# Optimization experiments

Measured on AMD Instinct MI355X. Metric: run time of the kernel, lower is better.

The kernel has to match this reference:

```python
import jax, jax.numpy as jnp
import numpy as np

N = 16777216  # batch*A*width*height (flat anchor-score vector)
BINS = 10
LOSS_WEIGHT = 1.0


def setup_inputs() -> dict:
    key = jax.random.key(0)
    k1, k2, k3 = jax.random.split(key, 3)
    pred = jax.random.normal(k1, (N,), dtype=jnp.float32)          # IoU logits
    target = jax.random.uniform(k2, (N,), dtype=jnp.float32)       # IoU targets in [0,1]
    label_weight = (jax.random.uniform(k3, (N,)) > 0.3).astype(jnp.float32)  # 1=valid, 0=ignore
    return {"pred": pred, "target": target, "label_weight": label_weight, "bins": BINS}


def reference(pred, target, label_weight, bins):
    # target is detached in the original module
    target = jax.lax.stop_gradient(target)
    # gradient norm g = |sigmoid(pred).detach() - target|, lies in [0,1]
    g = jnp.abs(jax.lax.stop_gradient(jax.nn.sigmoid(pred)) - target)
    valid = label_weight > 0
    validf = valid.astype(jnp.float32)
    tot = jnp.maximum(jnp.sum(validf), 1.0)

    # edges are i/bins with last edge nudged by 1e-6, so bin = floor(g*bins) clipped to bins-1
    bin_idx = jnp.clip((g * bins).astype(jnp.int32), 0, bins - 1)
    counts = jax.ops.segment_sum(validf, bin_idx, num_segments=bins)  # per-bin valid counts
    n = jnp.sum(counts > 0).astype(jnp.float32)                        # number of nonempty bins
    counts_safe = jnp.maximum(counts, 1.0)
    w_per_bin = jnp.where(counts > 0, tot / counts_safe, 0.0) / jnp.maximum(n, 1.0)
    weights = jnp.where(valid, w_per_bin[bin_idx], 0.0)

    # weighted BCE-with-logits, reduction='sum', stable form: logaddexp(0,x) - x*z
    bce = jnp.logaddexp(0.0, pred) - pred * target
    loss = jnp.sum(weights * bce) / tot
    return loss * LOSS_WEIGHT
```

## Files before the change

### kernel.cpp

```cpp
#include <hip/hip_runtime.h>

#define BINS 10
#define REPLICAS 16
#define NBLOCKS 2048
#define NTHREADS 256


typedef float vfloat4 __attribute__((ext_vector_type(4)));

__global__ __launch_bounds__(NTHREADS, 4)
void ghm_pass1(const float* __restrict__ pred,
               const float* __restrict__ target,
               const float* __restrict__ lw,
               float* __restrict__ rep_sums,
               unsigned int* __restrict__ rep_cnts,
               int n)
{
    __shared__ float ls[BINS];
    __shared__ unsigned int lc[BINS];
    if (threadIdx.x < BINS) { ls[threadIdx.x] = 0.0f; lc[threadIdx.x] = 0u; }

    float s0=0.f,s1=0.f,s2=0.f,s3=0.f,s4=0.f,s5=0.f,s6=0.f,s7=0.f,s8=0.f,s9=0.f;
    unsigned long long cpk = 0ull;

#define SBIN(B, S) { (S) += (bi_ == (B)) ? bce_ : 0.0f; }
#define PROC(P, T, W) do {                                                     \
    float p_ = (P), t_ = (T);                                                  \
    float ap_ = fabsf(p_);                                                     \
    float q_  = __builtin_amdgcn_exp2f(ap_ * -1.4426950408889634f); \
    float r_  = __builtin_amdgcn_rcpf(1.0f + q_);                              \
    float sig_ = (p_ >= 0.0f) ? r_ : (1.0f - r_);                              \
    float g_   = fabsf(sig_ - t_);                                             \
    int bi_ = (int)(g_ * 10.0f);                                               \
    bi_ = bi_ > 9 ? 9 : bi_;                                                   \
    bi_ = ((W) > 0.0f) ? bi_ : 10;              \
    float bce_ = fmaxf(p_, 0.0f)                                               \
               + 0.6931471805599453f * __builtin_amdgcn_logf(1.0f + q_)        \
               - p_ * t_;                                                      \
    cpk += 1ull << (6 * bi_);                                                  \
    SBIN(0,s0) SBIN(1,s1) SBIN(2,s2) SBIN(3,s3) SBIN(4,s4)                     \
    SBIN(5,s5) SBIN(6,s6) SBIN(7,s7) SBIN(8,s8) SBIN(9,s9)                     \
} while (0)
#define PROC4(PV, TV, WV) {                                                    \
    PROC((PV).x, (TV).x, (WV).x);                                              \
    PROC((PV).y, (TV).y, (WV).y);                                              \
    PROC((PV).z, (TV).z, (WV).z);                                              \
    PROC((PV).w, (TV).w, (WV).w); }

    const int n4 = n >> 2;
    const int full = n4 / (NBLOCKS * NTHREADS);
    const vfloat4* p4 = (const vfloat4*)pred;
    const vfloat4* t4 = (const vfloat4*)target;
    const vfloat4* w4 = (const vfloat4*)lw;
    const int gid = blockIdx.x * NTHREADS + threadIdx.x;
    const int stride = NBLOCKS * NTHREADS;

    if (full == 8) {
        const int base = blockIdx.x * 8 * NTHREADS + threadIdx.x;
#define LD(J, PB, TB, WB)                                                      \
        vfloat4 PB = __builtin_nontemporal_load(&p4[base + (J) * NTHREADS]);   \
        vfloat4 TB = __builtin_nontemporal_load(&t4[base + (J) * NTHREADS]);   \
        vfloat4 WB = __builtin_nontemporal_load(&w4[base + (J) * NTHREADS]);
        LD(0, P0, T0, W0) LD(1, P1, T1, W1) LD(2, P2, T2, W2) LD(3, P3, T3, W3)
        LD(4, P4, T4, W4) LD(5, P5, T5, W5) LD(6, P6, T6, W6) LD(7, P7, T7, W7)
        __builtin_amdgcn_sched_barrier(0);
        PROC4(P0, T0, W0);
        PROC4(P1, T1, W1);
        PROC4(P2, T2, W2);
        PROC4(P3, T3, W3);
        PROC4(P4, T4, W4);
        PROC4(P5, T5, W5);
        PROC4(P6, T6, W6);
        PROC4(P7, T7, W7);
#undef LD
    } else {
        if (full >= 2) {
            const int base = blockIdx.x * full * NTHREADS + threadIdx.x;
            vfloat4 pA = __builtin_nontemporal_load(&p4[base]);
            vfloat4 tA = __builtin_nontemporal_load(&t4[base]);
            vfloat4 wA = __builtin_nontemporal_load(&w4[base]);
            vfloat4 pB = __builtin_nontemporal_load(&p4[base + NTHREADS]);
            vfloat4 tB = __builtin_nontemporal_load(&t4[base + NTHREADS]);
            vfloat4 wB = __builtin_nontemporal_load(&w4[base + NTHREADS]);
            __builtin_amdgcn_sched_barrier(0);
            for (int j = 2; j < full; ++j) {
                const int idx = base + j * NTHREADS;
                vfloat4 pC = __builtin_nontemporal_load(&p4[idx]);
                vfloat4 tC = __builtin_nontemporal_load(&t4[idx]);
                vfloat4 wC = __builtin_nontemporal_load(&w4[idx]);
                __builtin_amdgcn_sched_barrier(0);
                PROC4(pA, tA, wA);
                pA = pB; tA = tB; wA = wB;
                pB = pC; tB = tC; wB = wC;
            }
            PROC4(pA, tA, wA);
            PROC4(pB, tB, wB);
        } else if (full == 1) {
            const int base = blockIdx.x * NTHREADS + threadIdx.x;
            vfloat4 pv = p4[base], tv = t4[base], wv = w4[base];
            PROC4(pv, tv, wv);
        }
        for (int i = full * stride + gid; i < n4; i += stride) {
            vfloat4 pv = p4[i], tv = t4[i], wv = w4[i];
            PROC4(pv, tv, wv);
        }
        for (int j = (n4 << 2) + gid; j < n; j += stride) {
            PROC(pred[j], target[j], lw[j]);
        }
    }

    unsigned int c0 = (unsigned int)(cpk       ) & 63u;
    unsigned int c1 = (unsigned int)(cpk >>  6 ) & 63u;
    unsigned int c2 = (unsigned int)(cpk >> 12 ) & 63u;
    unsigned int c3 = (unsigned int)(cpk >> 18 ) & 63u;
    unsigned int c4 = (unsigned int)(cpk >> 24 ) & 63u;
    unsigned int c5 = (unsigned int)(cpk >> 30 ) & 63u;
    unsigned int c6 = (unsigned int)(cpk >> 36 ) & 63u;
    unsigned int c7 = (unsigned int)(cpk >> 42 ) & 63u;
    unsigned int c8 = (unsigned int)(cpk >> 48 ) & 63u;
    unsigned int c9 = (unsigned int)(cpk >> 54 ) & 63u;

#define WREDUCE(S, C) {                                                        \
    _Pragma("unroll")                                                          \
    for (int o_ = 32; o_ > 0; o_ >>= 1) {                                      \
        (S) += __shfl_down((S), o_, 64);                                       \
        (C) += __shfl_down((C), o_, 64);                                       \
    } }
    WREDUCE(s0,c0) WREDUCE(s1,c1) WREDUCE(s2,c2) WREDUCE(s3,c3) WREDUCE(s4,c4)
    WREDUCE(s5,c5) WREDUCE(s6,c6) WREDUCE(s7,c7) WREDUCE(s8,c8) WREDUCE(s9,c9)

    __syncthreads();
    if ((threadIdx.x & 63) == 0) {
        atomicAdd(&ls[0], s0); atomicAdd(&lc[0], c0);
        atomicAdd(&ls[1], s1); atomicAdd(&lc[1], c1);
        atomicAdd(&ls[2], s2); atomicAdd(&lc[2], c2);
        atomicAdd(&ls[3], s3); atomicAdd(&lc[3], c3);
        atomicAdd(&ls[4], s4); atomicAdd(&lc[4], c4);
        atomicAdd(&ls[5], s5); atomicAdd(&lc[5], c5);
        atomicAdd(&ls[6], s6); atomicAdd(&lc[6], c6);
        atomicAdd(&ls[7], s7); atomicAdd(&lc[7], c7);
        atomicAdd(&ls[8], s8); atomicAdd(&lc[8], c8);
        atomicAdd(&ls[9], s9); atomicAdd(&lc[9], c9);
    }
    __syncthreads();
    if (threadIdx.x < BINS) {
        int rep = blockIdx.x & (REPLICAS - 1);
        atomicAdd(&rep_sums[rep * BINS + threadIdx.x], ls[threadIdx.x]);
        atomicAdd(&rep_cnts[rep * BINS + threadIdx.x], lc[threadIdx.x]);
    }
#undef PROC
#undef PROC4
#undef SBIN
#undef WREDUCE
}

__global__ void ghm_finalize(const float* __restrict__ rep_sums,
                             const unsigned int* __restrict__ rep_cnts,
                             float* __restrict__ out)
{
    __shared__ double S[BINS];
    __shared__ unsigned int C[BINS];
    int t = threadIdx.x;
    if (t < BINS) {
        double s = 0.0;
        unsigned int cc = 0u;
        for (int r = 0; r < REPLICAS; ++r) {
            s += (double)rep_sums[r * BINS + t];
            cc += rep_cnts[r * BINS + t];
        }
        S[t] = s;
        C[t] = cc;
    }
    __syncthreads();
    if (t == 0) {
        double n_ne = 0.0;
        for (int b = 0; b < BINS; ++b) if (C[b] > 0u) n_ne += 1.0;
        double nn = n_ne > 1.0 ? n_ne : 1.0;
        double loss = 0.0;
        for (int b = 0; b < BINS; ++b)
            if (C[b] > 0u) loss += S[b] / ((double)C[b] * nn);
        out[0] = (float)loss;
    }
}

extern "C" void kernel_launch(void* const* d_in, const int* in_sizes, int n_in,
                              void* d_out, int out_size, void* d_ws, size_t ws_size,
                              hipStream_t stream)
{
    const float* pred = (const float*)d_in[0];
    const float* target = (const float*)d_in[1];
    const float* lw = (const float*)d_in[2];
    int n = in_sizes[0];

    float* rep_sums = (float*)d_ws;
    unsigned int* rep_cnts =
        (unsigned int*)((char*)d_ws + REPLICAS * BINS * sizeof(float));

    (void)hipMemsetAsync(d_ws, 0, 2 * REPLICAS * BINS * sizeof(float), stream);
    ghm_pass1<<<NBLOCKS, NTHREADS, 0, stream>>>(pred, target, lw,
                                                rep_sums, rep_cnts, n);
    ghm_finalize<<<1, 64, 0, stream>>>(rep_sums, rep_cnts, (float*)d_out);
}
```

Measured before the change: 186.6 us.

## Replace register per-bin accumulators with replicated shared-memory atomic histogram

Each element no longer does ten predicated adds into per-bin register sums plus a packed 64-bit counter. It now issues LDS float atomics into a shared histogram replicated 16 ways by lane. The wave shuffle reductions go away, and the counts become floats, with the finalize kernel adjusted to match. The aim is to cut per-element ALU work and register pressure. The cost is two LDS atomics per valid element, with bank and replica contention (lanes 16 apart share a slot), and float counts lose exactness above 2^24 per slot.

```diff
diff --git a/kernel.cpp b/kernel.cpp
--- a/kernel.cpp
+++ b/kernel.cpp
@@ -1,6 +1,7 @@
 #include <hip/hip_runtime.h>
 
 #define BINS 10
+#define HREP 16
 #define REPLICAS 16
 #define NBLOCKS 2048
 #define NTHREADS 256
@@ -13,17 +14,19 @@
                const float* __restrict__ target,
                const float* __restrict__ lw,
                float* __restrict__ rep_sums,
-               unsigned int* __restrict__ rep_cnts,
+               float* __restrict__ rep_cnts,
                int n)
 {
-    __shared__ float ls[BINS];
-    __shared__ unsigned int lc[BINS];
-    if (threadIdx.x < BINS) { ls[threadIdx.x] = 0.0f; lc[threadIdx.x] = 0u; }
+    __shared__ float hsum[BINS * HREP];
+    __shared__ float hcnt[BINS * HREP];
+    if (threadIdx.x < BINS * HREP) {
+        hsum[threadIdx.x] = 0.0f;
+        hcnt[threadIdx.x] = 0.0f;
+    }
+    __syncthreads();
 
-    float s0=0.f,s1=0.f,s2=0.f,s3=0.f,s4=0.f,s5=0.f,s6=0.f,s7=0.f,s8=0.f,s9=0.f;
-    unsigned long long cpk = 0ull;
+    const int rep_ = threadIdx.x & (HREP - 1);
 
-#define SBIN(B, S) { (S) += (bi_ == (B)) ? bce_ : 0.0f; }
 #define PROC(P, T, W) do {                                                     \
     float p_ = (P), t_ = (T);                                                  \
     float ap_ = fabsf(p_);                                                     \
@@ -33,13 +36,14 @@
     float g_   = fabsf(sig_ - t_);                                             \
     int bi_ = (int)(g_ * 10.0f);                                               \
     bi_ = bi_ > 9 ? 9 : bi_;                                                   \
-    bi_ = ((W) > 0.0f) ? bi_ : 10;              \
     float bce_ = fmaxf(p_, 0.0f)                                               \
                + 0.6931471805599453f * __builtin_amdgcn_logf(1.0f + q_)        \
                - p_ * t_;                                                      \
-    cpk += 1ull << (6 * bi_);                                                  \
-    SBIN(0,s0) SBIN(1,s1) SBIN(2,s2) SBIN(3,s3) SBIN(4,s4)                     \
-    SBIN(5,s5) SBIN(6,s6) SBIN(7,s7) SBIN(8,s8) SBIN(9,s9)                     \
+    if ((W) > 0.0f) {                                                          \
+        int a_ = (bi_ << 4) + rep_;                                            \
+        atomicAdd(&hsum[a_], bce_);                 \
+        atomicAdd(&hcnt[a_], 1.0f);                                            \
+    }                                                                          \
 } while (0)
 #define PROC4(PV, TV, WV) {                                                    \
     PROC((PV).x, (TV).x, (WV).x);                                              \
@@ -109,64 +113,35 @@
         }
     }
 
-    unsigned int c0 = (unsigned int)(cpk       ) & 63u;
-    unsigned int c1 = (unsigned int)(cpk >>  6 ) & 63u;
-    unsigned int c2 = (unsigned int)(cpk >> 12 ) & 63u;
-    unsigned int c3 = (unsigned int)(cpk >> 18 ) & 63u;
-    unsigned int c4 = (unsigned int)(cpk >> 24 ) & 63u;
-    unsigned int c5 = (unsigned int)(cpk >> 30 ) & 63u;
-    unsigned int c6 = (unsigned int)(cpk >> 36 ) & 63u;
-    unsigned int c7 = (unsigned int)(cpk >> 42 ) & 63u;
-    unsigned int c8 = (unsigned int)(cpk >> 48 ) & 63u;
-    unsigned int c9 = (unsigned int)(cpk >> 54 ) & 63u;
-
-#define WREDUCE(S, C) {                                                        \
-    _Pragma("unroll")                                                          \
-    for (int o_ = 32; o_ > 0; o_ >>= 1) {                                      \
-        (S) += __shfl_down((S), o_, 64);                                       \
-        (C) += __shfl_down((C), o_, 64);                                       \
-    } }
-    WREDUCE(s0,c0) WREDUCE(s1,c1) WREDUCE(s2,c2) WREDUCE(s3,c3) WREDUCE(s4,c4)
-    WREDUCE(s5,c5) WREDUCE(s6,c6) WREDUCE(s7,c7) WREDUCE(s8,c8) WREDUCE(s9,c9)
-
-    __syncthreads();
-    if ((threadIdx.x & 63) == 0) {
-        atomicAdd(&ls[0], s0); atomicAdd(&lc[0], c0);
-        atomicAdd(&ls[1], s1); atomicAdd(&lc[1], c1);
-        atomicAdd(&ls[2], s2); atomicAdd(&lc[2], c2);
-        atomicAdd(&ls[3], s3); atomicAdd(&lc[3], c3);
-        atomicAdd(&ls[4], s4); atomicAdd(&lc[4], c4);
-        atomicAdd(&ls[5], s5); atomicAdd(&lc[5], c5);
-        atomicAdd(&ls[6], s6); atomicAdd(&lc[6], c6);
-        atomicAdd(&ls[7], s7); atomicAdd(&lc[7], c7);
-        atomicAdd(&ls[8], s8); atomicAdd(&lc[8], c8);
-        atomicAdd(&ls[9], s9); atomicAdd(&lc[9], c9);
-    }
     __syncthreads();
     if (threadIdx.x < BINS) {
+        float ssum = 0.0f, scnt = 0.0f;
+        const int b16 = threadIdx.x << 4;
+#pragma unroll
+        for (int r = 0; r < HREP; ++r) {
+            ssum += hsum[b16 + r];
+            scnt += hcnt[b16 + r];
+        }
         int rep = blockIdx.x & (REPLICAS - 1);
-        atomicAdd(&rep_sums[rep * BINS + threadIdx.x], ls[threadIdx.x]);
-        atomicAdd(&rep_cnts[rep * BINS + threadIdx.x], lc[threadIdx.x]);
+        atomicAdd(&rep_sums[rep * BINS + threadIdx.x], ssum);
+        atomicAdd(&rep_cnts[rep * BINS + threadIdx.x], scnt);
     }
 #undef PROC
 #undef PROC4
-#undef SBIN
-#undef WREDUCE
 }
 
 __global__ void ghm_finalize(const float* __restrict__ rep_sums,
-                             const unsigned int* __restrict__ rep_cnts,
+                             const float* __restrict__ rep_cnts,
                              float* __restrict__ out)
 {
     __shared__ double S[BINS];
-    __shared__ unsigned int C[BINS];
+    __shared__ double C[BINS];
     int t = threadIdx.x;
     if (t < BINS) {
-        double s = 0.0;
-        unsigned int cc = 0u;
+        double s = 0.0, cc = 0.0;
         for (int r = 0; r < REPLICAS; ++r) {
             s += (double)rep_sums[r * BINS + t];
-            cc += rep_cnts[r * BINS + t];
+            cc += (double)rep_cnts[r * BINS + t];
         }
         S[t] = s;
         C[t] = cc;
@@ -174,11 +149,11 @@
     __syncthreads();
     if (t == 0) {
         double n_ne = 0.0;
-        for (int b = 0; b < BINS; ++b) if (C[b] > 0u) n_ne += 1.0;
+        for (int b = 0; b < BINS; ++b) if (C[b] > 0.0) n_ne += 1.0;
         double nn = n_ne > 1.0 ? n_ne : 1.0;
         double loss = 0.0;
         for (int b = 0; b < BINS; ++b)
-            if (C[b] > 0u) loss += S[b] / ((double)C[b] * nn);
+            if (C[b] > 0.0) loss += S[b] / (C[b] * nn);
         out[0] = (float)loss;
     }
 }
@@ -193,8 +168,7 @@
     int n = in_sizes[0];
 
     float* rep_sums = (float*)d_ws;
-    unsigned int* rep_cnts =
-        (unsigned int*)((char*)d_ws + REPLICAS * BINS * sizeof(float));
+    float* rep_cnts = (float*)((char*)d_ws + REPLICAS * BINS * sizeof(float));
 
     (void)hipMemsetAsync(d_ws, 0, 2 * REPLICAS * BINS * sizeof(float), stream);
     ghm_pass1<<<NBLOCKS, NTHREADS, 0, stream>>>(pred, target, lw,
```

New measurement: 269.4 us. 1.44x slower.

## Replace register select-accumulate histogram with per-thread LDS rows updated by atomics

Applied to the files above, without the earlier changes.

Swaps the ten register accumulators (updated by compare-and-select for every element) and the packed 6-bit count word for a private 11-float-stride row per thread in shared memory, updated with LDS float atomicAdd for both sum and count. Counts become floats, and the finalize kernel reads them as doubles. The sigmoid gradient is also rewritten to pick the target side by sign instead of recomputing 1-r. The change trades ALU select work for two LDS atomics per element and about 22KB of LDS per block, which can lower occupancy and add LDS latency to a kernel that is memory-bound.

```diff
diff --git a/kernel.cpp b/kernel.cpp
--- a/kernel.cpp
+++ b/kernel.cpp
@@ -1,6 +1,7 @@
 #include <hip/hip_runtime.h>
 
 #define BINS 10
+#define ROWW 11
 #define REPLICAS 16
 #define NBLOCKS 2048
 #define NTHREADS 256
@@ -13,33 +14,36 @@
                const float* __restrict__ target,
                const float* __restrict__ lw,
                float* __restrict__ rep_sums,
-               unsigned int* __restrict__ rep_cnts,
+               float* __restrict__ rep_cnts,
                int n)
 {
+    __shared__ float hs[NTHREADS * ROWW];
+    __shared__ float hc[NTHREADS * ROWW];
     __shared__ float ls[BINS];
-    __shared__ unsigned int lc[BINS];
-    if (threadIdx.x < BINS) { ls[threadIdx.x] = 0.0f; lc[threadIdx.x] = 0u; }
-
-    float s0=0.f,s1=0.f,s2=0.f,s3=0.f,s4=0.f,s5=0.f,s6=0.f,s7=0.f,s8=0.f,s9=0.f;
-    unsigned long long cpk = 0ull;
-
-#define SBIN(B, S) { (S) += (bi_ == (B)) ? bce_ : 0.0f; }
+    __shared__ float lc[BINS];
+    {
+        const int row = threadIdx.x * ROWW;
+#pragma unroll
+        for (int b = 0; b < BINS; ++b) { hs[row + b] = 0.0f; hc[row + b] = 0.0f; }
+        if (threadIdx.x < BINS) { ls[threadIdx.x] = 0.0f; lc[threadIdx.x] = 0.0f; }
+    }
+    const int row_ = threadIdx.x * ROWW;
+
 #define PROC(P, T, W) do {                                                     \
     float p_ = (P), t_ = (T);                                                  \
     float ap_ = fabsf(p_);                                                     \
     float q_  = __builtin_amdgcn_exp2f(ap_ * -1.4426950408889634f); \
     float r_  = __builtin_amdgcn_rcpf(1.0f + q_);                              \
-    float sig_ = (p_ >= 0.0f) ? r_ : (1.0f - r_);                              \
-    float g_   = fabsf(sig_ - t_);                                             \
+    float tp_ = (p_ >= 0.0f) ? t_ : (1.0f - t_);         \
+    float g_  = fabsf(r_ - tp_);                                               \
     int bi_ = (int)(g_ * 10.0f);                                               \
     bi_ = bi_ > 9 ? 9 : bi_;                                                   \
-    bi_ = ((W) > 0.0f) ? bi_ : 10;              \
     float bce_ = fmaxf(p_, 0.0f)                                               \
                + 0.6931471805599453f * __builtin_amdgcn_logf(1.0f + q_)        \
                - p_ * t_;                                                      \
-    cpk += 1ull << (6 * bi_);                                                  \
-    SBIN(0,s0) SBIN(1,s1) SBIN(2,s2) SBIN(3,s3) SBIN(4,s4)                     \
-    SBIN(5,s5) SBIN(6,s6) SBIN(7,s7) SBIN(8,s8) SBIN(9,s9)                     \
+    float w01_ = ((W) > 0.0f) ? 1.0f : 0.0f;                                   \
+    atomicAdd(&hs[row_ + bi_], bce_ * w01_);    \
+    atomicAdd(&hc[row_ + bi_], w01_);                                          \
 } while (0)
 #define PROC4(PV, TV, WV) {                                                    \
     PROC((PV).x, (TV).x, (WV).x);                                              \
@@ -109,16 +113,12 @@
         }
     }
 
-    unsigned int c0 = (unsigned int)(cpk       ) & 63u;
-    unsigned int c1 = (unsigned int)(cpk >>  6 ) & 63u;
-    unsigned int c2 = (unsigned int)(cpk >> 12 ) & 63u;
-    unsigned int c3 = (unsigned int)(cpk >> 18 ) & 63u;
-    unsigned int c4 = (unsigned int)(cpk >> 24 ) & 63u;
-    unsigned int c5 = (unsigned int)(cpk >> 30 ) & 63u;
-    unsigned int c6 = (unsigned int)(cpk >> 36 ) & 63u;
-    unsigned int c7 = (unsigned int)(cpk >> 42 ) & 63u;
-    unsigned int c8 = (unsigned int)(cpk >> 48 ) & 63u;
-    unsigned int c9 = (unsigned int)(cpk >> 54 ) & 63u;
+    float s0 = hs[row_+0], s1 = hs[row_+1], s2 = hs[row_+2], s3 = hs[row_+3];
+    float s4 = hs[row_+4], s5 = hs[row_+5], s6 = hs[row_+6], s7 = hs[row_+7];
+    float s8 = hs[row_+8], s9 = hs[row_+9];
+    float c0 = hc[row_+0], c1 = hc[row_+1], c2 = hc[row_+2], c3 = hc[row_+3];
+    float c4 = hc[row_+4], c5 = hc[row_+5], c6 = hc[row_+6], c7 = hc[row_+7];
+    float c8 = hc[row_+8], c9 = hc[row_+9];
 
 #define WREDUCE(S, C) {                                                        \
     _Pragma("unroll")                                                          \
@@ -150,23 +150,21 @@
     }
 #undef PROC
 #undef PROC4
-#undef SBIN
 #undef WREDUCE
 }
 
 __global__ void ghm_finalize(const float* __restrict__ rep_sums,
-                             const unsigned int* __restrict__ rep_cnts,
+                             const float* __restrict__ rep_cnts,
                              float* __restrict__ out)
 {
     __shared__ double S[BINS];
-    __shared__ unsigned int C[BINS];
+    __shared__ double C[BINS];
     int t = threadIdx.x;
     if (t < BINS) {
-        double s = 0.0;
-        unsigned int cc = 0u;
+        double s = 0.0, cc = 0.0;
         for (int r = 0; r < REPLICAS; ++r) {
             s += (double)rep_sums[r * BINS + t];
-            cc += rep_cnts[r * BINS + t];
+            cc += (double)rep_cnts[r * BINS + t];
         }
         S[t] = s;
         C[t] = cc;
@@ -174,11 +172,11 @@
     __syncthreads();
     if (t == 0) {
         double n_ne = 0.0;
-        for (int b = 0; b < BINS; ++b) if (C[b] > 0u) n_ne += 1.0;
+        for (int b = 0; b < BINS; ++b) if (C[b] > 0.0) n_ne += 1.0;
         double nn = n_ne > 1.0 ? n_ne : 1.0;
         double loss = 0.0;
         for (int b = 0; b < BINS; ++b)
-            if (C[b] > 0u) loss += S[b] / ((double)C[b] * nn);
+            if (C[b] > 0.0) loss += S[b] / (C[b] * nn);
         out[0] = (float)loss;
     }
 }
@@ -193,8 +191,7 @@
     int n = in_sizes[0];
 
     float* rep_sums = (float*)d_ws;
-    unsigned int* rep_cnts =
-        (unsigned int*)((char*)d_ws + REPLICAS * BINS * sizeof(float));
+    float* rep_cnts = (float*)((char*)d_ws + REPLICAS * BINS * sizeof(float));
 
     (void)hipMemsetAsync(d_ws, 0, 2 * REPLICAS * BINS * sizeof(float), stream);
     ghm_pass1<<<NBLOCKS, NTHREADS, 0, stream>>>(pred, target, lw,
```

Measured after the change: 330.6 us. +77.2%, slower.
